# Performance work log

Measured on AMD Instinct MI355X. Metric: run time of the kernel, lower is better.

The kernel has to match this reference:

```python
import jax, jax.numpy as jnp
import numpy as np

N_PIECES = 4
N_ACTIONS = 4
H = W = 4


def _conv3x3(x, w, b):
    # x: [B,C,H,W], w: [O,C,3,3] (torch OIHW), padding=1
    y = jax.lax.conv_general_dilated(x, w, window_strides=(1, 1), padding=((1, 1), (1, 1)),
                                     dimension_numbers=('NCHW', 'OIHW', 'NCHW'))
    return y + b[None, :, None, None]


def _conv1x1(x, w, b):
    # 1x1 conv as einsum; w: [O,C,1,1]
    return jnp.einsum('bchw,oc->bohw', x, w[:, :, 0, 0]) + b[None, :, None, None]


def setup_inputs() -> dict:
    key = jax.random.key(0)
    ks = jax.random.split(key, 20)
    B = 131072
    ob = jax.random.randint(ks[0], (B, H, W), 0, N_PIECES)
    ac = jax.random.randint(ks[1], (B,), 0, N_ACTIONS)

    def rnd(k, shape, fan_in):
        bound = 1.0 / np.sqrt(fan_in)
        return jax.random.uniform(k, shape, jnp.float32, -bound, bound)

    p = {}
    p['w_start1'] = rnd(ks[2], (32, N_PIECES + N_ACTIONS, 3, 3), 8 * 9)
    p['b_start1'] = rnd(ks[3], (32,), 8 * 9)
    p['w_start2'] = rnd(ks[4], (16, 32, 1, 1), 32)
    p['b_start2'] = rnd(ks[5], (16,), 32)
    p['w_ob1'] = rnd(ks[6], (16, 16, 1, 1), 16)
    p['b_ob1'] = rnd(ks[7], (16,), 16)
    p['w_ob2'] = rnd(ks[8], (N_PIECES * 2, 16 + N_PIECES, 1, 1), 20)
    p['b_ob2'] = rnd(ks[9], (N_PIECES * 2,), 20)
    p['w_reward'] = rnd(ks[10], (8, 16, 1, 1), 16)
    p['b_reward'] = rnd(ks[11], (8,), 16)
    p['fc_reward_w'] = rnd(ks[12], (4, 8 * H * W), 8 * H * W)
    p['fc_reward_b'] = rnd(ks[13], (4,), 8 * H * W)
    p['w_go'] = rnd(ks[14], (8, 16, 1, 1), 16)
    p['b_go'] = rnd(ks[15], (8,), 16)
    p['fc_go_w'] = rnd(ks[16], (4, 8 * H * W), 8 * H * W)
    p['fc_go_b'] = rnd(ks[17], (4,), 8 * H * W)
    return {'ob': ob, 'ac': ac, **p}


def reference(ob, ac, w_start1, b_start1, w_start2, b_start2, w_ob1, b_ob1, w_ob2, b_ob2,
              w_reward, b_reward, fc_reward_w, fc_reward_b, w_go, b_go, fc_go_w, fc_go_b):
    B = ob.shape[0]
    # one-hot encode board and action
    ob_oh = (ob[:, None, :, :] == jnp.arange(N_PIECES)[None, :, None, None]).astype(jnp.float32)  # [B,4,4,4]
    ac_oh = (ac[:, None] == jnp.arange(N_ACTIONS)[None, :]).astype(jnp.float32)  # [B,4]
    ac_map = jnp.broadcast_to(ac_oh[:, :, None, None], (B, N_ACTIONS, H, W))
    x = jnp.concatenate([ob_oh, ac_map], axis=1)  # [B,8,4,4]

    x = jax.nn.relu(_conv3x3(x, w_start1, b_start1))
    x = jax.nn.relu(_conv1x1(x, w_start2, b_start2))  # [B,16,4,4]

    # next-ob head
    nol = jax.nn.relu(_conv1x1(x, w_ob1, b_ob1))
    nol = jnp.concatenate([nol, ob_oh], axis=1)  # [B,20,4,4]
    nol = _conv1x1(nol, w_ob2, b_ob2)  # [B,8,4,4]
    nol = jnp.transpose(nol, (0, 2, 3, 1))  # [B,4,4,8]
    next_ob_loc = nol[..., :N_PIECES]
    next_ob_scale = nol[..., N_PIECES:]

    # reward head
    r = jax.nn.relu(_conv1x1(x, w_reward, b_reward)).reshape(B, -1)
    r = r @ fc_reward_w.T + fc_reward_b
    reward_loc, reward_scale = r[:, :2], r[:, 2:]

    # game-over head
    g = jax.nn.relu(_conv1x1(x, w_go, b_go)).reshape(B, -1)
    g = g @ fc_go_w.T + fc_go_b
    go_loc, go_scale = g[:, :2], g[:, 2:]

    return (next_ob_loc, next_ob_scale, reward_loc, reward_scale, go_loc, go_scale)
```

## Files before the change

kernel.cpp:

```cpp
#include <hip/hip_runtime.h>
#include <hip/hip_bf16.h>

typedef unsigned short u16;
typedef unsigned int u32;
typedef unsigned long long u64;

typedef _Float16 vh8 __attribute__((ext_vector_type(8)));
typedef _Float16 hv2 __attribute__((ext_vector_type(2)));
typedef __attribute__((ext_vector_type(16))) float vf16;

#define A1_OFF   0
#define A2_OFF   1280
#define A3_OFF   2048
#define A4_OFF   2560
#define FH_OFF   3072
#define FB_OFF   4096
#define FLAG_OFF 4104

__device__ __forceinline__ float bf2f(u16 h){ union{u32 u; float f;} v; v.u=((u32)h)<<16; return v.f; }
__device__ __forceinline__ u16 f2h(float f){ _Float16 h=(_Float16)f; return __builtin_bit_cast(u16,h); }
__device__ __forceinline__ float ldw(const void* p,int i,bool bf){ return bf? bf2f(((const u16*)p)[i]) : ((const float*)p)[i]; }

__device__ __forceinline__ bool detect_bf16(const void* w1){
  const u16* p=(const u16*)w1; bool ok=true;
  for(int k=0;k<64;++k){ float v=bf2f(p[k]); ok &= (fabsf(v)<=0.125f); }
  return ok;
}

__device__ __constant__ int PI[32] = {0,1,2,3,8,9,10,11,4,5,6,7,12,13,14,15,
                                      16,17,18,19,24,25,26,27,20,21,22,23,28,29,30,31};

__global__ __launch_bounds__(256) void dw_prep(
    const void* w1, const void* b1, const void* w2, const void* b2,
    const void* wo1, const void* bo1, const void* wo2, const void* bo2,
    const void* wr, const void* br, const void* fcr, const void* fbr,
    const void* wg, const void* bg, const void* fcg, const void* fbg,
    u32* wsu){
  const int tid = threadIdx.x;
  const bool bf = detect_bf16(w1);
  float* wsf = (float*)wsu;

  for (int t=tid; t<1280; t+=256){
    int kb=t>>8, l=(t>>2)&63, r=t&3, hi=l>>5, row=l&31;
    u32 w=0;
    for (int u=0;u<2;++u){
      int m=2*r+u, tt=m>>2, q=m&3, s=2*kb+tt;
      int pos = (s<5)? (2*s+hi) : (2*(s-5)+hi);
      float v=0.f;
      if (pos<=8){
        if (s<5) v = ldw(w1, row*72 + q*9 + pos, bf);
        else {
          v = ldw(w1, row*72 + (4+q)*9 + pos, bf);
          if (pos==4) v += ldw(b1, row, bf);
        }
      }
      w |= ((u32)f2h(v)) << (16*u);
    }
    wsu[A1_OFF+t]=w;
  }
  for (int t=tid; t<768; t+=256){
    int kb=t>>8, l=(t>>2)&63, r=t&3, hi=l>>5, row=l&31;
    int K0=kb*16+hi*8+2*r; u32 w=0;
    for (int s=0;s<2;++s){
      int K=K0+s; float v=0.f;
      if (K<32){ if(row<16) v=ldw(w2, row*32+PI[K], bf); }
      else if (K==32 && row<16) v=ldw(b2, row, bf);
      w |= ((u32)f2h(v)) << (16*s);
    }
    wsu[A2_OFF+t]=w;
  }
  for (int t=tid; t<512; t+=256){
    int kb=t>>8, l=(t>>2)&63, r=t&3, hi=l>>5, row=l&31;
    int K0=kb*16+hi*8+2*r; u32 w=0;
    for (int s=0;s<2;++s){
      int K=K0+s; float v=0.f;
      if (K<16){
        int c=PI[K];
        v = (row<16)? ldw(wo1,row*16+c,bf) : (row<24)? ldw(wr,(row-16)*16+c,bf) : ldw(wg,(row-24)*16+c,bf);
      } else if (K==16){
        v = (row<16)? ldw(bo1,row,bf) : (row<24)? ldw(br,row-16,bf) : ldw(bg,row-24,bf);
      }
      w |= ((u32)f2h(v)) << (16*s);
    }
    wsu[A3_OFF+t]=w;
  }
  for (int t=tid; t<512; t+=256){
    int kb=t>>8, l=(t>>2)&63, r=t&3, hi=l>>5, row=l&31;
    int K0=kb*16+hi*8+2*r; u32 w=0;
    for (int s=0;s<2;++s){
      int K=K0+s; float v=0.f;
      if (row<8){
        if (K<16)              v=ldw(wo2, row*20+PI[K], bf);
        else if (K==16)        v=ldw(bo2, row, bf);
        else if (K>=17&&K<=20) v=ldw(wo2, row*20+16+(K-17), bf);
      }
      w |= ((u32)f2h(v)) << (16*s);
    }
    wsu[A4_OFF+t]=w;
  }
  for (int t=tid; t<512; t+=256){
    int head=t>>8, r=t&255, hi=r>>7, c16=(r>>3)&15, k=(r>>1)&3, j=r&1;
    const void* f = head ? fcg : fcr;
    float v0 = ldw(f, k*128+(4*hi+2*j)*16+c16, bf);
    float v1 = ldw(f, k*128+(4*hi+2*j+1)*16+c16, bf);
    wsu[FH_OFF+t] = (u32)f2h(v0) | ((u32)f2h(v1)<<16);
  }
  for (int t=tid; t<8; t+=256) wsf[FB_OFF+t] = ldw(t<4?fbr:fbg, t&3, bf);
  if (tid==0) wsu[FLAG_OFF] = bf ? 1u : 0u;
}

__host__ __device__ constexpr u32 nbpgen(int c, int hi){
  u32 v=0;
  for (int s=0;s<5;++s){
    int pos=2*s+hi; u32 f=32;
    if (pos<=8){
      int ni=c/4+pos/3-1, nj=c%4+pos%3-1;
      if (ni>=0&&ni<4&&nj>=0&&nj<4) f=(u32)((ni*4+nj)<<1);
    }
    v |= f << (6*s);
  }
  return v;
}
__device__ __constant__ u32 NBP[32] = {
  nbpgen(0,0),nbpgen(1,0),nbpgen(2,0),nbpgen(3,0),nbpgen(4,0),nbpgen(5,0),nbpgen(6,0),nbpgen(7,0),
  nbpgen(8,0),nbpgen(9,0),nbpgen(10,0),nbpgen(11,0),nbpgen(12,0),nbpgen(13,0),nbpgen(14,0),nbpgen(15,0),
  nbpgen(0,1),nbpgen(1,1),nbpgen(2,1),nbpgen(3,1),nbpgen(4,1),nbpgen(5,1),nbpgen(6,1),nbpgen(7,1),
  nbpgen(8,1),nbpgen(9,1),nbpgen(10,1),nbpgen(11,1),nbpgen(12,1),nbpgen(13,1),nbpgen(14,1),nbpgen(15,1)};

__device__ __forceinline__ vf16 mfma(int4 a, int4 b, vf16 c){
  union{int4 i; vh8 v;} ua, ub; ua.i=a; ub.i=b;
  return __builtin_amdgcn_mfma_f32_32x32x16_f16(ua.v, ub.v, c, 0, 0, 0);
}
__device__ __forceinline__ u32 pkh(float a, float b){
#if __has_builtin(__builtin_amdgcn_cvt_pkrtz)
  auto h = __builtin_amdgcn_cvt_pkrtz(a, b);
  return __builtin_bit_cast(u32, h);
#else
  return (u32)f2h(a) | ((u32)f2h(b)<<16);
#endif
}
__device__ __forceinline__ u32 pkmax0(u32 x){
  u32 d; asm("v_pk_max_f16 %0, %1, 0" : "=v"(d) : "v"(x)); return d;
}
__device__ __forceinline__ float dot2(u32 w, u32 x, float c){
#if __has_builtin(__builtin_amdgcn_fdot2)
  return __builtin_amdgcn_fdot2(__builtin_bit_cast(hv2,w), __builtin_bit_cast(hv2,x), c, false);
#else
  hv2 a=__builtin_bit_cast(hv2,w), b=__builtin_bit_cast(hv2,x);
  return c + (float)a[0]*(float)b[0] + (float)a[1]*(float)b[1];
#endif
}
__device__ __forceinline__ u32 pkbf(float a, float b){
  u16 lo=__builtin_bit_cast(u16,__float2bfloat16(a));
  u16 hi=__builtin_bit_cast(u16,__float2bfloat16(b));
  return (u32)lo | ((u32)hi<<16);
}
template<int CTRL> __device__ __forceinline__ float dppadd(float x){
  int y=__builtin_amdgcn_update_dpp(0,__builtin_bit_cast(int,x),CTRL,0xF,0xF,false);
  return x+__builtin_bit_cast(float,y);
}
template<int CTRL> __device__ __forceinline__ u32 dppor(u32 x){
  u32 y=(u32)__builtin_amdgcn_update_dpp(0,(int)x,CTRL,0xF,0xF,false);
  return x|y;
}
template<int CTRL> __device__ __forceinline__ float dppmov(float x){
  int y=__builtin_amdgcn_update_dpp(0,__builtin_bit_cast(int,x),CTRL,0xF,0xF,false);
  return __builtin_bit_cast(float,y);
}

__global__ __launch_bounds__(256) void dw_main(
    const int* __restrict__ ob, const int* __restrict__ ac,
    const u32* __restrict__ g, void* __restrict__ outp, int B){
  __shared__ int4 sW4[576];
  const int4* gA = (const int4*)g;

  const int tid  = threadIdx.x;
#pragma unroll
  for (int i=0;i<3;++i){
    int t = tid + (i<<8);
    if (t < 576) sW4[t] = gA[320 + t];
  }
  __syncthreads();

  const int lane = tid & 63;
  const int hi   = lane >> 5;
  const int col  = lane & 31;
  const int c16  = col & 15;
  const int elem = col >> 4;
  const int wid  = tid >> 6;
  const bool obf = g[FLAG_OFF] != 0u;
  const float* gS = (const float*)g;

  const int e = (int)(blockIdx.x<<3) + (wid<<1) + elem;
  const bool act = (e < B);
  const int eL = act ? e : 0;

  const u32 nbp = NBP[(hi<<4)|c16];
  const int4 bconst = make_int4(hi?0:0x3C00, 0, 0, 0);
  const vf16 zero = {0.f,0.f,0.f,0.f,0.f,0.f,0.f,0.f,0.f,0.f,0.f,0.f,0.f,0.f,0.f,0.f};
  const int xaddr = (lane^32)<<2;

  u32 pkv = ((u32)ob[(size_t)eL*16 + c16]) << (c16<<1);
  pkv = dppor<0x121>(pkv);
  pkv = dppor<0x122>(pkv);
  pkv = dppor<0x124>(pkv);
  pkv = dppor<0x128>(pkv);
  const int a = ac[eL];

  int4 A1f[5];
#pragma unroll
  for (int kb=0;kb<5;++kb) A1f[kb]=gA[(A1_OFF>>2)+kb*64+lane];

  u64 ohA = 0x3C00ull << (a<<4);
  const u32 ohA_lo=(u32)ohA, ohA_hi=(u32)(ohA>>32);
  int4 breg[5];
#pragma unroll
  for (int kb=0;kb<5;++kb){
    u32 w[4];
#pragma unroll
    for (int t=0;t<2;++t){
      const int s = kb*2+t;
      u32 w0, w1;
      if (s < 5){
        u32 v = (nbp >> (6*s)) & 63u;
        u32 np = (pkv >> (v & 31u)) & 3u;
        u32 src = (v < 32u) ? 0x3C00u : 0u;
        u64 oh = (u64)src << (np << 4);
        w0=(u32)oh; w1=(u32)(oh>>32);
      } else {
        u32 inval = (nbp >> (6*(s-5))) & 32u;
        w0 = inval ? 0u : ohA_lo;
        w1 = inval ? 0u : ohA_hi;
      }
      w[2*t]=w0; w[2*t+1]=w1;
    }
    breg[kb]=make_int4(w[0],w[1],w[2],w[3]);
  }

  vf16 acc = zero;
#pragma unroll
  for (int kb=0;kb<5;++kb) acc = mfma(A1f[kb], breg[kb], acc);

  int4 A2f[3];
#pragma unroll
  for (int kb=0;kb<3;++kb) A2f[kb]=sW4[kb*64+lane];
  u32 zh[8];
#pragma unroll
  for (int i=0;i<8;++i) zh[i]=pkmax0(pkh(acc[2*i], acc[2*i+1]));
  vf16 acc2 = mfma(A2f[0], make_int4(zh[0],zh[1],zh[2],zh[3]), zero);
  acc2 = mfma(A2f[1], make_int4(zh[4],zh[5],zh[6],zh[7]), acc2);
  acc2 = mfma(A2f[2], bconst, acc2);

  int4 A3f[2];
#pragma unroll
  for (int kb=0;kb<2;++kb) A3f[kb]=sW4[192+kb*64+lane];
  u32 xh[4];
#pragma unroll
  for (int i=0;i<4;++i) xh[i]=pkmax0(pkh(acc2[2*i], acc2[2*i+1]));
  vf16 acc3 = mfma(A3f[0], make_int4(xh[0],xh[1],xh[2],xh[3]), zero);
  acc3 = mfma(A3f[1], bconst, acc3);

  int4 A4f[2];
#pragma unroll
  for (int kb=0;kb<2;++kb) A4f[kb]=sW4[320+kb*64+lane];
  u32 nh[4];
#pragma unroll
  for (int i=0;i<4;++i) nh[i]=pkmax0(pkh(acc3[2*i], acc3[2*i+1]));
  const int p = (int)((pkv >> (c16<<1)) & 3u);
  u64 t64 = 0x3C00ull << (p<<4);
  u32 t_lo=(u32)t64, t_hi=(u32)(t64>>32);
  u32 pb0 = 0x3C00u | (t_lo<<16);
  u32 pb1 = (t_lo>>16) | (t_hi<<16);
  u32 pb2 = t_hi>>16;
  int4 B4b = make_int4(hi?0u:pb0, hi?0u:pb1, hi?0u:pb2, 0u);
  vf16 acc4 = mfma(A4f[0], make_int4(nh[0],nh[1],nh[2],nh[3]), zero);
  acc4 = mfma(A4f[1], B4b, acc4);

  if (act){
    size_t bofs=(size_t)e*64 + c16*4;
    size_t off = hi ? ((size_t)B*64 + bofs) : bofs;
    if (obf){
      u16* o16=(u16*)outp;
      *(uint2*)(o16+off) = make_uint2(pkbf(acc4[0],acc4[1]), pkbf(acc4[2],acc4[3]));
    } else {
      float* of=(float*)outp;
      *(float4*)(of+off) = make_float4(acc4[0],acc4[1],acc4[2],acc4[3]);
    }
  }

  u32 ra01 = pkmax0(pkh(acc3[8],  acc3[9]));
  u32 ra23 = pkmax0(pkh(acc3[10], acc3[11]));
  u32 ga01 = pkmax0(pkh(acc3[12], acc3[13]));
  u32 ga23 = pkmax0(pkh(acc3[14], acc3[15]));
  int4 tr0 = sW4[448 + hi*32 + c16*2];
  int4 tr1 = sW4[448 + hi*32 + c16*2 + 1];
  int4 tg0 = sW4[448 + 64 + hi*32 + c16*2];
  int4 tg1 = sW4[448 + 64 + hi*32 + c16*2 + 1];
  float rk[4], gk[4];
  rk[0] = dot2((u32)tr0.x, ra01, dot2((u32)tr0.y, ra23, 0.f));
  rk[1] = dot2((u32)tr0.z, ra01, dot2((u32)tr0.w, ra23, 0.f));
  rk[2] = dot2((u32)tr1.x, ra01, dot2((u32)tr1.y, ra23, 0.f));
  rk[3] = dot2((u32)tr1.z, ra01, dot2((u32)tr1.w, ra23, 0.f));
  gk[0] = dot2((u32)tg0.x, ga01, dot2((u32)tg0.y, ga23, 0.f));
  gk[1] = dot2((u32)tg0.z, ga01, dot2((u32)tg0.w, ga23, 0.f));
  gk[2] = dot2((u32)tg1.x, ga01, dot2((u32)tg1.y, ga23, 0.f));
  gk[3] = dot2((u32)tg1.z, ga01, dot2((u32)tg1.w, ga23, 0.f));

  const bool b0 = (c16&1), b1 = ((c16>>1)&1);
  float pr, pg;
  {
#pragma unroll
    for (int k=0;k<4;++k){ rk[k]=dppadd<0xB1>(rk[k]); gk[k]=dppadd<0xB1>(gk[k]); }
    float rp = b0 ? rk[2] : rk[0], rq = b0 ? rk[3] : rk[1];
    float gp = b0 ? gk[2] : gk[0], gq = b0 ? gk[3] : gk[1];
    rp=dppadd<0x4E>(rp); rq=dppadd<0x4E>(rq);
    gp=dppadd<0x4E>(gp); gq=dppadd<0x4E>(gq);
    pr = b1 ? rq : rp;
    pg = b1 ? gq : gp;
    pr=dppadd<0x124>(pr); pr=dppadd<0x128>(pr);
    pg=dppadd<0x124>(pg); pg=dppadd<0x128>(pg);
    int yr=__builtin_amdgcn_ds_bpermute(xaddr,__builtin_bit_cast(int,pr));
    int yg=__builtin_amdgcn_ds_bpermute(xaddr,__builtin_bit_cast(int,pg));
    pr += __builtin_bit_cast(float,yr);
    pg += __builtin_bit_cast(float,yg);
  }
  float yr2 = dppmov<0x4E>(pr);
  float yg2 = dppmov<0x4E>(pg);
  if (act && hi==0 && c16<2){
    float fb0 = gS[FB_OFF + (c16<<1)];
    float fb1 = gS[FB_OFF + (c16<<1)+1];
    float fb2 = gS[FB_OFF + 4 + (c16<<1)];
    float fb3 = gS[FB_OFF + 4 + (c16<<1)+1];
    if (obf){
      u32* o32=(u32*)outp;
      o32[(size_t)B*64 + (size_t)c16*B + e]     = pkbf(pr+fb0, yr2+fb1);
      o32[(size_t)B*64 + (size_t)(2+c16)*B + e] = pkbf(pg+fb2, yg2+fb3);
    } else {
      float* of=(float*)outp;
      *(float2*)(of + (size_t)B*128 + (size_t)c16*2*B + (size_t)e*2)     = make_float2(pr+fb0, yr2+fb1);
      *(float2*)(of + (size_t)B*128 + (size_t)(2+c16)*2*B + (size_t)e*2) = make_float2(pg+fb2, yg2+fb3);
    }
  }
}

extern "C" void kernel_launch(void* const* d_in, const int* in_sizes, int n_in,
                              void* d_out, int out_size, void* d_ws, size_t ws_size,
                              hipStream_t stream) {
  const int* ob = (const int*)d_in[0];
  const int* ac = (const int*)d_in[1];
  u32* ws = (u32*)d_ws;
  const int B = in_sizes[1];

  hipLaunchKernelGGL(dw_prep, dim3(1), dim3(256), 0, stream,
                     d_in[2], d_in[3], d_in[4], d_in[5], d_in[6], d_in[7],
                     d_in[8], d_in[9], d_in[10], d_in[11], d_in[12], d_in[13],
                     d_in[14], d_in[15], d_in[16], d_in[17], ws);

  const int nb = (B + 7) / 8;
  hipLaunchKernelGGL(dw_main, dim3(nb), dim3(256), 0, stream, ob, ac, ws, d_out, B);
}
```

Baseline: 51.06 us.

## Precompute action conv contribution as lookup table; process two elements per wave

The action one-hot channels of the 3x3 conv, plus the bias, are folded into a precomputed per-action, per-position table in the prep kernel. The main kernel loads this table into LDS and uses it to initialise the accumulator, which drops two of the five first-layer MFMAs. Each wave now handles two element pairs in sequence, halving the grid and amortising the LDS weight staging. The cost is extra LDS for the table and more per-thread work, which could reduce occupancy or latency hiding.

```diff
diff --git a/kernel.cpp b/kernel.cpp
--- a/kernel.cpp
+++ b/kernel.cpp
@@ -16,6 +16,7 @@
 #define FH_OFF   3072
 #define FB_OFF   4096
 #define FLAG_OFF 4104
+#define T_OFF    4160
 
 __device__ __forceinline__ float bf2f(u16 h){ union{u32 u; float f;} v; v.u=((u32)h)<<16; return v.f; }
 __device__ __forceinline__ u16 f2h(float f){ _Float16 h=(_Float16)f; return __builtin_bit_cast(u16,h); }
@@ -40,23 +41,30 @@
   const bool bf = detect_bf16(w1);
   float* wsf = (float*)wsu;
 
-  for (int t=tid; t<1280; t+=256){
+  for (int t=tid; t<768; t+=256){
     int kb=t>>8, l=(t>>2)&63, r=t&3, hi=l>>5, row=l&31;
     u32 w=0;
     for (int u=0;u<2;++u){
       int m=2*r+u, tt=m>>2, q=m&3, s=2*kb+tt;
-      int pos = (s<5)? (2*s+hi) : (2*(s-5)+hi);
+      int pos = 2*s+hi;
       float v=0.f;
-      if (pos<=8){
-        if (s<5) v = ldw(w1, row*72 + q*9 + pos, bf);
-        else {
-          v = ldw(w1, row*72 + (4+q)*9 + pos, bf);
-          if (pos==4) v += ldw(b1, row, bf);
-        }
-      }
+      if (s<5 && pos<=8) v = ldw(w1, row*72 + q*9 + pos, bf);
       w |= ((u32)f2h(v)) << (16*u);
     }
     wsu[A1_OFF+t]=w;
+  }
+  for (int t=tid; t<2048; t+=256){
+    int a=t>>9, hi=(t>>8)&1, rq=(t>>6)&3, c16=(t>>2)&15, rl=t&3;
+    int row = rl + 8*rq + 4*hi;
+    int ci=c16>>2, cj=c16&3;
+    float s0 = ldw(b1, row, bf);
+    for (int dy=0; dy<3; ++dy)
+      for (int dx=0; dx<3; ++dx){
+        int ni=ci+dy-1, nj=cj+dx-1;
+        if (ni>=0&&ni<4&&nj>=0&&nj<4)
+          s0 += ldw(w1, row*72 + (4+a)*9 + dy*3+dx, bf);
+      }
+    wsf[T_OFF+t] = s0;
   }
   for (int t=tid; t<768; t+=256){
     int kb=t>>8, l=(t>>2)&63, r=t&3, hi=l>>5, row=l&31;
@@ -172,14 +180,16 @@
     const int* __restrict__ ob, const int* __restrict__ ac,
     const u32* __restrict__ g, void* __restrict__ outp, int B){
   __shared__ int4 sW4[576];
+  __shared__ float4 sT4[512];
   const int4* gA = (const int4*)g;
+  const float4* gT = (const float4*)g;
 
   const int tid  = threadIdx.x;
-#pragma unroll
-  for (int i=0;i<3;++i){
-    int t = tid + (i<<8);
-    if (t < 576) sW4[t] = gA[320 + t];
-  }
+  sW4[tid] = gA[320+tid];
+  sW4[tid+256] = gA[320+tid+256];
+  if (tid < 64) sW4[tid+512] = gA[320+tid+512];
+  sT4[tid] = gT[(T_OFF>>2)+tid];
+  sT4[tid+256] = gT[(T_OFF>>2)+tid+256];
   __syncthreads();
 
   const int lane = tid & 63;
@@ -191,156 +201,148 @@
   const bool obf = g[FLAG_OFF] != 0u;
   const float* gS = (const float*)g;
 
-  const int e = (int)(blockIdx.x<<3) + (wid<<1) + elem;
-  const bool act = (e < B);
-  const int eL = act ? e : 0;
-
   const u32 nbp = NBP[(hi<<4)|c16];
   const int4 bconst = make_int4(hi?0:0x3C00, 0, 0, 0);
   const vf16 zero = {0.f,0.f,0.f,0.f,0.f,0.f,0.f,0.f,0.f,0.f,0.f,0.f,0.f,0.f,0.f,0.f};
   const int xaddr = (lane^32)<<2;
 
-  u32 pkv = ((u32)ob[(size_t)eL*16 + c16]) << (c16<<1);
-  pkv = dppor<0x121>(pkv);
-  pkv = dppor<0x122>(pkv);
-  pkv = dppor<0x124>(pkv);
-  pkv = dppor<0x128>(pkv);
-  const int a = ac[eL];
-
-  int4 A1f[5];
-#pragma unroll
-  for (int kb=0;kb<5;++kb) A1f[kb]=gA[(A1_OFF>>2)+kb*64+lane];
-
-  u64 ohA = 0x3C00ull << (a<<4);
-  const u32 ohA_lo=(u32)ohA, ohA_hi=(u32)(ohA>>32);
-  int4 breg[5];
-#pragma unroll
-  for (int kb=0;kb<5;++kb){
-    u32 w[4];
-#pragma unroll
-    for (int t=0;t<2;++t){
-      const int s = kb*2+t;
-      u32 w0, w1;
-      if (s < 5){
-        u32 v = (nbp >> (6*s)) & 63u;
-        u32 np = (pkv >> (v & 31u)) & 3u;
-        u32 src = (v < 32u) ? 0x3C00u : 0u;
-        u64 oh = (u64)src << (np << 4);
-        w0=(u32)oh; w1=(u32)(oh>>32);
+  const int eA = (int)(blockIdx.x<<4) + (wid<<2) + elem;
+
+  auto chain = [&](int e){
+    const bool act = (e < B);
+    const int eL = act ? e : 0;
+
+    u32 pkv = ((u32)ob[(size_t)eL*16 + c16]) << (c16<<1);
+    pkv = dppor<0x121>(pkv);
+    pkv = dppor<0x122>(pkv);
+    pkv = dppor<0x124>(pkv);
+    pkv = dppor<0x128>(pkv);
+    const int a = ac[eL];
+
+    int4 breg[3];
+#pragma unroll
+    for (int kb=0;kb<3;++kb){
+      u32 w[4];
+#pragma unroll
+      for (int t=0;t<2;++t){
+        const int s = kb*2+t;
+        u32 w0=0, w1=0;
+        if (s < 5){
+          u32 v = (nbp >> (6*s)) & 63u;
+          u32 np = (pkv >> (v & 31u)) & 3u;
+          u32 src = (v < 32u) ? 0x3C00u : 0u;
+          u64 oh = (u64)src << (np << 4);
+          w0=(u32)oh; w1=(u32)(oh>>32);
+        }
+        w[2*t]=w0; w[2*t+1]=w1;
+      }
+      breg[kb]=make_int4(w[0],w[1],w[2],w[3]);
+    }
+
+    vf16 acc;
+#pragma unroll
+    for (int rq=0;rq<4;++rq){
+      float4 q = sT4[(a*8 + hi*4 + rq)*16 + c16];
+      acc[4*rq+0]=q.x; acc[4*rq+1]=q.y; acc[4*rq+2]=q.z; acc[4*rq+3]=q.w;
+    }
+#pragma unroll
+    for (int kb=0;kb<3;++kb) acc = mfma(gA[(A1_OFF>>2)+kb*64+lane], breg[kb], acc);
+
+    u32 zh[8];
+#pragma unroll
+    for (int i=0;i<8;++i) zh[i]=pkmax0(pkh(acc[2*i], acc[2*i+1]));
+    vf16 acc2 = mfma(sW4[lane], make_int4(zh[0],zh[1],zh[2],zh[3]), zero);
+    acc2 = mfma(sW4[64+lane], make_int4(zh[4],zh[5],zh[6],zh[7]), acc2);
+    acc2 = mfma(sW4[128+lane], bconst, acc2);
+
+    u32 xh[4];
+#pragma unroll
+    for (int i=0;i<4;++i) xh[i]=pkmax0(pkh(acc2[2*i], acc2[2*i+1]));
+    vf16 acc3 = mfma(sW4[192+lane], make_int4(xh[0],xh[1],xh[2],xh[3]), zero);
+    acc3 = mfma(sW4[256+lane], bconst, acc3);
+
+    u32 nh[4];
+#pragma unroll
+    for (int i=0;i<4;++i) nh[i]=pkmax0(pkh(acc3[2*i], acc3[2*i+1]));
+    const int p = (int)((pkv >> (c16<<1)) & 3u);
+    u64 t64 = 0x3C00ull << (p<<4);
+    u32 t_lo=(u32)t64, t_hi=(u32)(t64>>32);
+    u32 pb0 = 0x3C00u | (t_lo<<16);
+    u32 pb1 = (t_lo>>16) | (t_hi<<16);
+    u32 pb2 = t_hi>>16;
+    int4 B4b = make_int4(hi?0u:pb0, hi?0u:pb1, hi?0u:pb2, 0u);
+    vf16 acc4 = mfma(sW4[320+lane], make_int4(nh[0],nh[1],nh[2],nh[3]), zero);
+    acc4 = mfma(sW4[384+lane], B4b, acc4);
+
+    if (act){
+      size_t bofs=(size_t)e*64 + c16*4;
+      size_t off = hi ? ((size_t)B*64 + bofs) : bofs;
+      if (obf){
+        u16* o16=(u16*)outp;
+        *(uint2*)(o16+off) = make_uint2(pkbf(acc4[0],acc4[1]), pkbf(acc4[2],acc4[3]));
       } else {
-        u32 inval = (nbp >> (6*(s-5))) & 32u;
-        w0 = inval ? 0u : ohA_lo;
-        w1 = inval ? 0u : ohA_hi;
-      }
-      w[2*t]=w0; w[2*t+1]=w1;
-    }
-    breg[kb]=make_int4(w[0],w[1],w[2],w[3]);
-  }
-
-  vf16 acc = zero;
-#pragma unroll
-  for (int kb=0;kb<5;++kb) acc = mfma(A1f[kb], breg[kb], acc);
-
-  int4 A2f[3];
-#pragma unroll
-  for (int kb=0;kb<3;++kb) A2f[kb]=sW4[kb*64+lane];
-  u32 zh[8];
-#pragma unroll
-  for (int i=0;i<8;++i) zh[i]=pkmax0(pkh(acc[2*i], acc[2*i+1]));
-  vf16 acc2 = mfma(A2f[0], make_int4(zh[0],zh[1],zh[2],zh[3]), zero);
-  acc2 = mfma(A2f[1], make_int4(zh[4],zh[5],zh[6],zh[7]), acc2);
-  acc2 = mfma(A2f[2], bconst, acc2);
-
-  int4 A3f[2];
-#pragma unroll
-  for (int kb=0;kb<2;++kb) A3f[kb]=sW4[192+kb*64+lane];
-  u32 xh[4];
-#pragma unroll
-  for (int i=0;i<4;++i) xh[i]=pkmax0(pkh(acc2[2*i], acc2[2*i+1]));
-  vf16 acc3 = mfma(A3f[0], make_int4(xh[0],xh[1],xh[2],xh[3]), zero);
-  acc3 = mfma(A3f[1], bconst, acc3);
-
-  int4 A4f[2];
-#pragma unroll
-  for (int kb=0;kb<2;++kb) A4f[kb]=sW4[320+kb*64+lane];
-  u32 nh[4];
-#pragma unroll
-  for (int i=0;i<4;++i) nh[i]=pkmax0(pkh(acc3[2*i], acc3[2*i+1]));
-  const int p = (int)((pkv >> (c16<<1)) & 3u);
-  u64 t64 = 0x3C00ull << (p<<4);
-  u32 t_lo=(u32)t64, t_hi=(u32)(t64>>32);
-  u32 pb0 = 0x3C00u | (t_lo<<16);
-  u32 pb1 = (t_lo>>16) | (t_hi<<16);
-  u32 pb2 = t_hi>>16;
-  int4 B4b = make_int4(hi?0u:pb0, hi?0u:pb1, hi?0u:pb2, 0u);
-  vf16 acc4 = mfma(A4f[0], make_int4(nh[0],nh[1],nh[2],nh[3]), zero);
-  acc4 = mfma(A4f[1], B4b, acc4);
-
-  if (act){
-    size_t bofs=(size_t)e*64 + c16*4;
-    size_t off = hi ? ((size_t)B*64 + bofs) : bofs;
-    if (obf){
-      u16* o16=(u16*)outp;
-      *(uint2*)(o16+off) = make_uint2(pkbf(acc4[0],acc4[1]), pkbf(acc4[2],acc4[3]));
-    } else {
-      float* of=(float*)outp;
-      *(float4*)(of+off) = make_float4(acc4[0],acc4[1],acc4[2],acc4[3]);
-    }
-  }
-
-  u32 ra01 = pkmax0(pkh(acc3[8],  acc3[9]));
-  u32 ra23 = pkmax0(pkh(acc3[10], acc3[11]));
-  u32 ga01 = pkmax0(pkh(acc3[12], acc3[13]));
-  u32 ga23 = pkmax0(pkh(acc3[14], acc3[15]));
-  int4 tr0 = sW4[448 + hi*32 + c16*2];
-  int4 tr1 = sW4[448 + hi*32 + c16*2 + 1];
-  int4 tg0 = sW4[448 + 64 + hi*32 + c16*2];
-  int4 tg1 = sW4[448 + 64 + hi*32 + c16*2 + 1];
-  float rk[4], gk[4];
-  rk[0] = dot2((u32)tr0.x, ra01, dot2((u32)tr0.y, ra23, 0.f));
-  rk[1] = dot2((u32)tr0.z, ra01, dot2((u32)tr0.w, ra23, 0.f));
-  rk[2] = dot2((u32)tr1.x, ra01, dot2((u32)tr1.y, ra23, 0.f));
-  rk[3] = dot2((u32)tr1.z, ra01, dot2((u32)tr1.w, ra23, 0.f));
-  gk[0] = dot2((u32)tg0.x, ga01, dot2((u32)tg0.y, ga23, 0.f));
-  gk[1] = dot2((u32)tg0.z, ga01, dot2((u32)tg0.w, ga23, 0.f));
-  gk[2] = dot2((u32)tg1.x, ga01, dot2((u32)tg1.y, ga23, 0.f));
-  gk[3] = dot2((u32)tg1.z, ga01, dot2((u32)tg1.w, ga23, 0.f));
-
-  const bool b0 = (c16&1), b1 = ((c16>>1)&1);
-  float pr, pg;
-  {
-#pragma unroll
-    for (int k=0;k<4;++k){ rk[k]=dppadd<0xB1>(rk[k]); gk[k]=dppadd<0xB1>(gk[k]); }
-    float rp = b0 ? rk[2] : rk[0], rq = b0 ? rk[3] : rk[1];
-    float gp = b0 ? gk[2] : gk[0], gq = b0 ? gk[3] : gk[1];
-    rp=dppadd<0x4E>(rp); rq=dppadd<0x4E>(rq);
-    gp=dppadd<0x4E>(gp); gq=dppadd<0x4E>(gq);
-    pr = b1 ? rq : rp;
-    pg = b1 ? gq : gp;
-    pr=dppadd<0x124>(pr); pr=dppadd<0x128>(pr);
-    pg=dppadd<0x124>(pg); pg=dppadd<0x128>(pg);
-    int yr=__builtin_amdgcn_ds_bpermute(xaddr,__builtin_bit_cast(int,pr));
-    int yg=__builtin_amdgcn_ds_bpermute(xaddr,__builtin_bit_cast(int,pg));
-    pr += __builtin_bit_cast(float,yr);
-    pg += __builtin_bit_cast(float,yg);
-  }
-  float yr2 = dppmov<0x4E>(pr);
-  float yg2 = dppmov<0x4E>(pg);
-  if (act && hi==0 && c16<2){
-    float fb0 = gS[FB_OFF + (c16<<1)];
-    float fb1 = gS[FB_OFF + (c16<<1)+1];
-    float fb2 = gS[FB_OFF + 4 + (c16<<1)];
-    float fb3 = gS[FB_OFF + 4 + (c16<<1)+1];
-    if (obf){
-      u32* o32=(u32*)outp;
-      o32[(size_t)B*64 + (size_t)c16*B + e]     = pkbf(pr+fb0, yr2+fb1);
-      o32[(size_t)B*64 + (size_t)(2+c16)*B + e] = pkbf(pg+fb2, yg2+fb3);
-    } else {
-      float* of=(float*)outp;
-      *(float2*)(of + (size_t)B*128 + (size_t)c16*2*B + (size_t)e*2)     = make_float2(pr+fb0, yr2+fb1);
-      *(float2*)(of + (size_t)B*128 + (size_t)(2+c16)*2*B + (size_t)e*2) = make_float2(pg+fb2, yg2+fb3);
-    }
-  }
+        float* of=(float*)outp;
+        *(float4*)(of+off) = make_float4(acc4[0],acc4[1],acc4[2],acc4[3]);
+      }
+    }
+
+    u32 ra01 = pkmax0(pkh(acc3[8],  acc3[9]));
+    u32 ra23 = pkmax0(pkh(acc3[10], acc3[11]));
+    u32 ga01 = pkmax0(pkh(acc3[12], acc3[13]));
+    u32 ga23 = pkmax0(pkh(acc3[14], acc3[15]));
+    int4 tr0 = sW4[448 + hi*32 + c16*2];
+    int4 tr1 = sW4[448 + hi*32 + c16*2 + 1];
+    int4 tg0 = sW4[448 + 64 + hi*32 + c16*2];
+    int4 tg1 = sW4[448 + 64 + hi*32 + c16*2 + 1];
+    float rk[4], gk[4];
+    rk[0] = dot2((u32)tr0.x, ra01, dot2((u32)tr0.y, ra23, 0.f));
+    rk[1] = dot2((u32)tr0.z, ra01, dot2((u32)tr0.w, ra23, 0.f));
+    rk[2] = dot2((u32)tr1.x, ra01, dot2((u32)tr1.y, ra23, 0.f));
+    rk[3] = dot2((u32)tr1.z, ra01, dot2((u32)tr1.w, ra23, 0.f));
+    gk[0] = dot2((u32)tg0.x, ga01, dot2((u32)tg0.y, ga23, 0.f));
+    gk[1] = dot2((u32)tg0.z, ga01, dot2((u32)tg0.w, ga23, 0.f));
+    gk[2] = dot2((u32)tg1.x, ga01, dot2((u32)tg1.y, ga23, 0.f));
+    gk[3] = dot2((u32)tg1.z, ga01, dot2((u32)tg1.w, ga23, 0.f));
+
+    const bool b0 = (c16&1), b1 = ((c16>>1)&1);
+    float pr, pg;
+    {
+#pragma unroll
+      for (int k=0;k<4;++k){ rk[k]=dppadd<0xB1>(rk[k]); gk[k]=dppadd<0xB1>(gk[k]); }
+      float rp = b0 ? rk[2] : rk[0], rq = b0 ? rk[3] : rk[1];
+      float gp = b0 ? gk[2] : gk[0], gq = b0 ? gk[3] : gk[1];
+      rp=dppadd<0x4E>(rp); rq=dppadd<0x4E>(rq);
+      gp=dppadd<0x4E>(gp); gq=dppadd<0x4E>(gq);
+      pr = b1 ? rq : rp;
+      pg = b1 ? gq : gp;
+      pr=dppadd<0x124>(pr); pr=dppadd<0x128>(pr);
+      pg=dppadd<0x124>(pg); pg=dppadd<0x128>(pg);
+      int yr=__builtin_amdgcn_ds_bpermute(xaddr,__builtin_bit_cast(int,pr));
+      int yg=__builtin_amdgcn_ds_bpermute(xaddr,__builtin_bit_cast(int,pg));
+      pr += __builtin_bit_cast(float,yr);
+      pg += __builtin_bit_cast(float,yg);
+    }
+    float yr2 = dppmov<0x4E>(pr);
+    float yg2 = dppmov<0x4E>(pg);
+    if (act && hi==0 && c16<2){
+      float fb0 = gS[FB_OFF + (c16<<1)];
+      float fb1 = gS[FB_OFF + (c16<<1)+1];
+      float fb2 = gS[FB_OFF + 4 + (c16<<1)];
+      float fb3 = gS[FB_OFF + 4 + (c16<<1)+1];
+      if (obf){
+        u32* o32=(u32*)outp;
+        o32[(size_t)B*64 + (size_t)c16*B + e]     = pkbf(pr+fb0, yr2+fb1);
+        o32[(size_t)B*64 + (size_t)(2+c16)*B + e] = pkbf(pg+fb2, yg2+fb3);
+      } else {
+        float* of=(float*)outp;
+        *(float2*)(of + (size_t)B*128 + (size_t)c16*2*B + (size_t)e*2)     = make_float2(pr+fb0, yr2+fb1);
+        *(float2*)(of + (size_t)B*128 + (size_t)(2+c16)*2*B + (size_t)e*2) = make_float2(pg+fb2, yg2+fb3);
+      }
+    }
+  };
+
+  chain(eA);
+  chain(eA + 2);
 }
 
 extern "C" void kernel_launch(void* const* d_in, const int* in_sizes, int n_in,
@@ -356,6 +358,6 @@
                      d_in[8], d_in[9], d_in[10], d_in[11], d_in[12], d_in[13],
                      d_in[14], d_in[15], d_in[16], d_in[17], ws);
 
-  const int nb = (B + 7) / 8;
+  const int nb = (B + 15) / 16;
   hipLaunchKernelGGL(dw_main, dim3(nb), dim3(256), 0, stream, ob, ac, ws, d_out, B);
 }
```

Result: slower. 59.81 us (+17.1%).
